# Optimization experiments

Hardware: AMD Instinct MI355X
Metric: run time of the kernel (lower is better)

Reference implementation:

```python
import jax, jax.numpy as jnp
import numpy as np

N = 100000
NEG_SLOPE = 0.2

def _leaky_relu(x, slope):
    return jnp.where(x >= 0, x, slope * x)

def _gat_layer(h_in, W, a_src, a_dst, b, src, dst, heads, out_ch):
    # h: [N, H, C]
    h = (h_in @ W).reshape(-1, heads, out_ch)
    alpha_src = (h * a_src).sum(-1)  # [N, H]
    alpha_dst = (h * a_dst).sum(-1)  # [N, H]
    e = _leaky_relu(alpha_src[src] + alpha_dst[dst], NEG_SLOPE)  # [E, H]
    # segment softmax over destination nodes
    m = jax.ops.segment_max(e, dst, num_segments=N)
    m = jnp.where(jnp.isfinite(m), m, 0.0)
    ex = jnp.exp(e - m[dst])
    denom = jax.ops.segment_sum(ex, dst, num_segments=N)
    attn = ex / (denom[dst] + 1e-16)  # [E, H]
    out = jax.ops.segment_sum(h[src] * attn[:, :, None], dst, num_segments=N)  # [N, H, C]
    return out.reshape(-1, heads * out_ch) + b

def setup_inputs() -> dict:
    key = jax.random.key(0)
    ks = jax.random.split(key, 10)
    F_in, H1, C1, n_cls = 512, 8, 8, 16
    E = 1600000
    x = jax.random.normal(ks[0], (N, F_in), dtype=jnp.float32)
    edge_index = jax.random.randint(ks[1], (2, E), 0, N, dtype=jnp.int64)
    s1 = 1.0 / np.sqrt(F_in)
    W1 = jax.random.uniform(ks[2], (F_in, H1 * C1), jnp.float32, -s1, s1)
    a1_src = jax.random.normal(ks[3], (H1, C1), dtype=jnp.float32) * 0.1
    a1_dst = jax.random.normal(ks[4], (H1, C1), dtype=jnp.float32) * 0.1
    b1 = jnp.zeros((H1 * C1,), jnp.float32)
    s2 = 1.0 / np.sqrt(H1 * C1)
    W2 = jax.random.uniform(ks[5], (H1 * C1, n_cls), jnp.float32, -s2, s2)
    a2_src = jax.random.normal(ks[6], (1, n_cls), dtype=jnp.float32) * 0.1
    a2_dst = jax.random.normal(ks[7], (1, n_cls), dtype=jnp.float32) * 0.1
    b2 = jnp.zeros((n_cls,), jnp.float32)
    return {"x": x, "edge_index": edge_index, "W1": W1, "a1_src": a1_src,
            "a1_dst": a1_dst, "b1": b1, "W2": W2, "a2_src": a2_src,
            "a2_dst": a2_dst, "b2": b2}

def reference(x, edge_index, W1, a1_src, a1_dst, b1, W2, a2_src, a2_dst, b2):
    # add self loops (GATConv default)
    loops = jnp.arange(N, dtype=edge_index.dtype)
    src = jnp.concatenate([edge_index[0], loops])
    dst = jnp.concatenate([edge_index[1], loops])
    h = _gat_layer(x, W1, a1_src, a1_dst, b1, src, dst, 8, 8)
    h = jax.nn.elu(h)
    out = _gat_layer(h, W2, a2_src, a2_dst, b2, src, dst, 1, 16)
    return jax.nn.log_softmax(out, axis=1)
```

## Files before the change

kernel.cpp:

```cpp
#include <hip/hip_runtime.h>
#include <math.h>

#define NEG_SLOPE 0.2f
#define BKT_SHIFT 8
#define BKT_RANGE 256
#define EPB 4096

typedef __attribute__((ext_vector_type(8))) short bf16x8;
typedef __attribute__((ext_vector_type(4))) float f32x4;

__device__ __forceinline__ float elu1(float x)  { return x > 0.f ? x : expm1f(x); }

__device__ __forceinline__ unsigned short f2bf(float f) {
  unsigned u = __float_as_uint(f);
  unsigned r = (u + 0x7FFFu + ((u >> 16) & 1u)) >> 16;
  return (unsigned short)r;
}
__device__ __forceinline__ float bflo(unsigned u) { return __uint_as_float(u << 16); }
__device__ __forceinline__ float bfhi(unsigned u) { return __uint_as_float(u & 0xFFFF0000u); }
__device__ __forceinline__ unsigned cvt_pk_bf16(float lo, float hi) {
  unsigned r;
  asm("v_cvt_pk_bf16_f32 %0, %1, %2" : "=v"(r) : "v"(lo), "v"(hi));
  return r;
}

__global__ __launch_bounds__(256) void k_cvtW_zero(const float* __restrict__ W,
                                                   unsigned short* __restrict__ Wt,
                                                   int* __restrict__ bucketCount) {
  int i = blockIdx.x * 256 + threadIdx.x;
  if (i < 1024) bucketCount[i] = 0;
  if (i >= 512 * 64) return;
  int k = i >> 6, c = i & 63;
  Wt[(size_t)c * 512 + k] = f2bf(W[i]);
}

__global__ __launch_bounds__(256) void k_gemm1_mfma(const float* __restrict__ x,
                                                    const unsigned short* __restrict__ Wt,
                                                    const float* __restrict__ a1s,
                                                    const float* __restrict__ a1d,
                                                    unsigned* __restrict__ hx,
                                                    unsigned* __restrict__ ef1dp, int N) {
  __shared__ __align__(16) float Sm[64 * 64];
  unsigned short* Bs = (unsigned short*)Sm;
  float* Asf = Sm;
  const int t = threadIdx.x;
  const int w = t >> 6;
  const int l = t & 63;
  const int fr = l & 15;
  const int fq = l >> 4;
  const int rowbase = blockIdx.x * 128;
  f32x4 acc[2][4] = {};

  const int r0g = rowbase + w * 32 + fr;
  const int r1g = r0g + 16;
  const bool v0 = r0g < N, v1 = r1g < N;
  const float* xr0 = x + (size_t)r0g * 512 + fq * 8;
  const float* xr1 = x + (size_t)r1g * 512 + fq * 8;

  for (int k0 = 0; k0 < 512; k0 += 64) {
#pragma unroll
    for (int rep = 0; rep < 2; ++rep) {
      int i = t + rep * 256;
      int c = i >> 3, ch = i & 7;
      uint4 v = *(const uint4*)(Wt + (size_t)c * 512 + k0 + ch * 8);
      *((uint4*)(Bs + c * 64 + (ch ^ (c & 7)) * 8)) = v;
    }
    bf16x8 a[2][2];
#pragma unroll
    for (int m = 0; m < 2; ++m) {
      const float* xr = m ? xr1 : xr0;
      bool vv = m ? v1 : v0;
#pragma unroll
      for (int ks = 0; ks < 2; ++ks) {
        float4 f0 = make_float4(0.f, 0.f, 0.f, 0.f), f1 = f0;
        if (vv) {
          f0 = *(const float4*)(xr + k0 + ks * 32);
          f1 = *(const float4*)(xr + k0 + ks * 32 + 4);
        }
        union { unsigned u[4]; bf16x8 v8; } un;
        un.u[0] = cvt_pk_bf16(f0.x, f0.y);
        un.u[1] = cvt_pk_bf16(f0.z, f0.w);
        un.u[2] = cvt_pk_bf16(f1.x, f1.y);
        un.u[3] = cvt_pk_bf16(f1.z, f1.w);
        a[m][ks] = un.v8;
      }
    }
    __syncthreads();
#pragma unroll
    for (int ks = 0; ks < 2; ++ks) {
      bf16x8 b[4];
#pragma unroll
      for (int n = 0; n < 4; ++n) {
        int c = n * 16 + fr;
        int ch = (ks * 4 + fq) ^ (c & 7);
        b[n] = *((const bf16x8*)(Bs + c * 64 + ch * 8));
      }
#pragma unroll
      for (int m = 0; m < 2; ++m)
#pragma unroll
        for (int n = 0; n < 4; ++n)
          acc[m][n] = __builtin_amdgcn_mfma_f32_16x16x32_bf16(a[m][ks], b[n], acc[m][n], 0, 0, 0);
    }
    __syncthreads();
  }

#pragma unroll
  for (int m = 0; m < 2; ++m) {
    if (m) __syncthreads();
#pragma unroll
    for (int reg = 0; reg < 4; ++reg) {
      int lrow = w * 16 + fq * 4 + reg;
#pragma unroll
      for (int n = 0; n < 4; ++n)
        Asf[lrow * 64 + n * 16 + fr] = acc[m][n][reg];
    }
    __syncthreads();
#pragma unroll
    for (int p = 0; p < 4; ++p) {
      int flat = p * 256 + t;
      int lrow = flat >> 4, j = flat & 15;
      int g = rowbase + ((lrow >> 4) << 5) + m * 16 + (lrow & 15);
      float4 f = *(float4*)(Asf + lrow * 64 + j * 4);
      unsigned u = __builtin_amdgcn_cvt_pk_fp8_f32(f.x, f.y, 0u, 0);
      u = __builtin_amdgcn_cvt_pk_fp8_f32(f.z, f.w, u, 1);
      if (g < N) hx[(size_t)g * 24 + 8 + j] = u;
    }
#pragma unroll
    for (int p = 0; p < 2; ++p) {
      int flat = p * 256 + t;
      int lrow = flat >> 3, hh = flat & 7;
      int g = rowbase + ((lrow >> 4) << 5) + m * 16 + (lrow & 15);
      float4 f0 = *(float4*)(Asf + lrow * 64 + hh * 8);
      float4 f1 = *(float4*)(Asf + lrow * 64 + hh * 8 + 4);
      const float* sa = a1s + hh * 8;
      const float* da = a1d + hh * 8;
      float ss = f0.x*sa[0]+f0.y*sa[1]+f0.z*sa[2]+f0.w*sa[3]
               + f1.x*sa[4]+f1.y*sa[5]+f1.z*sa[6]+f1.w*sa[7];
      float dd = f0.x*da[0]+f0.y*da[1]+f0.z*da[2]+f0.w*da[3]
               + f1.x*da[4]+f1.y*da[5]+f1.z*da[6]+f1.w*da[7];
      if (g < N) {
        hx[(size_t)g * 24 + hh] = cvt_pk_bf16(expf(ss), expf(NEG_SLOPE * ss));
        ef1dp[(size_t)g * 8 + hh] = cvt_pk_bf16(expf(dd), expf(NEG_SLOPE * dd));
      }
    }
  }
}

__global__ __launch_bounds__(256) void k_bhist(const int* __restrict__ dst,
                                               int* __restrict__ bucketCount,
                                               int E, int B) {
  __shared__ int h[512];
  int t = threadIdx.x;
  for (int i = t; i < B; i += 256) h[i] = 0;
  __syncthreads();
  int e0 = blockIdx.x * EPB;
#pragma unroll
  for (int i = 0; i < EPB / 256; ++i) {
    int e = e0 + i * 256 + t;
    if (e < E) atomicAdd(&h[dst[e] >> BKT_SHIFT], 1);
  }
  __syncthreads();
  for (int i = t; i < B; i += 256)
    if (h[i]) atomicAdd(bucketCount + i, h[i]);
}

__global__ __launch_bounds__(256) void k_bin(const int* __restrict__ src,
                                             const int* __restrict__ dst,
                                             const int* __restrict__ bucketCount,
                                             int* __restrict__ gCursorRel,
                                             unsigned* __restrict__ binned,
                                             int E, int B) {
  __shared__ int sc[512];
  __shared__ int hist[512];
  __shared__ int base[512];
  int t = threadIdx.x;
  sc[t]       = (t < B) ? bucketCount[t] : 0;
  sc[t + 256] = (t + 256 < B) ? bucketCount[t + 256] : 0;
  for (int i = t; i < 512; i += 256) hist[i] = 0;
  __syncthreads();
  for (int o = 1; o < 512; o <<= 1) {
    int a0 = (t >= o) ? sc[t - o] : 0;
    int a1 = (t + 256 >= o) ? sc[t + 256 - o] : 0;
    __syncthreads();
    sc[t] += a0;
    sc[t + 256] += a1;
    __syncthreads();
  }
  int e0 = blockIdx.x * EPB;
#pragma unroll
  for (int i = 0; i < EPB / 256; ++i) {
    int e = e0 + i * 256 + t;
    if (e < E) atomicAdd(&hist[dst[e] >> BKT_SHIFT], 1);
  }
  __syncthreads();
  for (int i = t; i < B; i += 256) {
    int c = hist[i];
    int excl = sc[i] - bucketCount[i];
    base[i] = c ? (excl + atomicAdd(gCursorRel + i, c)) : 0;
    hist[i] = 0;
  }
  __syncthreads();
#pragma unroll
  for (int i = 0; i < EPB / 256; ++i) {
    int e = e0 + i * 256 + t;
    if (e < E) {
      int d = dst[e];
      int b = d >> BKT_SHIFT;
      int r = atomicAdd(&hist[b], 1);
      binned[base[b] + r] = ((unsigned)(d & (BKT_RANGE - 1)) << 24) | (unsigned)src[e];
    }
  }
}

__global__ __launch_bounds__(256) void k_build(const int* __restrict__ bucketCount,
                                               const unsigned* __restrict__ binned,
                                               int* __restrict__ rowptr,
                                               int* __restrict__ deg,
                                               int* __restrict__ srt, int N, int B) {
  __shared__ int sc[512];
  __shared__ int ldeg[BKT_RANGE];
  __shared__ int sm[BKT_RANGE];
  __shared__ int lcur[BKT_RANGE];
  int t = threadIdx.x;
  int b = blockIdx.x;
  sc[t]       = (t < B) ? bucketCount[t] : 0;
  sc[t + 256] = (t + 256 < B) ? bucketCount[t + 256] : 0;
  ldeg[t] = 0;
  __syncthreads();
  for (int o = 1; o < 512; o <<= 1) {
    int a0 = (t >= o) ? sc[t - o] : 0;
    int a1 = (t + 256 >= o) ? sc[t + 256 - o] : 0;
    __syncthreads();
    sc[t] += a0;
    sc[t + 256] += a1;
    __syncthreads();
  }
  int eend = sc[b];
  int estart = eend - bucketCount[b];
  int nbase = b * BKT_RANGE;
  for (int e = estart + t; e < eend; e += 256)
    atomicAdd(&ldeg[binned[e] >> 24], 1);
  __syncthreads();
  int v = ldeg[t];
  sm[t] = v;
  __syncthreads();
  int acc = v;
#pragma unroll
  for (int o = 1; o < 256; o <<= 1) {
    int u = (t >= o) ? sm[t - o] : 0;
    __syncthreads();
    acc += u;
    sm[t] = acc;
    __syncthreads();
  }
  int excl = estart + acc - v;
  int node = nbase + t;
  if (node < N) {
    rowptr[node] = excl;
    deg[node] = v;
  }
  lcur[t] = excl;
  __syncthreads();
  for (int e = estart + t; e < eend; e += 256) {
    unsigned p = binned[e];
    int pos = atomicAdd(&lcur[p >> 24], 1);
    srt[pos] = (int)(p & 0xFFFFFFu);
  }
}

__global__ __launch_bounds__(256) void k_agg1f(const int* __restrict__ rowptr,
                                               const int* __restrict__ deg,
                                               const int* __restrict__ srt,
                                               const unsigned* __restrict__ hx,
                                               const unsigned* __restrict__ ef1dp,
                                               const float* __restrict__ b1,
                                               const float* __restrict__ W2,
                                               const float* __restrict__ a2s,
                                               const float* __restrict__ a2d,
                                               unsigned short* __restrict__ h2b,
                                               unsigned* __restrict__ ef2sp,
                                               float* __restrict__ ef2d, int N) {
  __shared__ float vsm[4][64];
  const int t = threadIdx.x;
  const int w = t >> 6;
  const int lane = t & 63;
  const int wid = blockIdx.x * 4 + w;
  const int slot = lane >> 4;
  const int c4 = lane & 15;
  const int h = c4 >> 1;
  float a2sr = a2s[c4];
  float a2dr = a2d[c4];
  float wreg[16];
#pragma unroll
  for (int m = 0; m < 16; ++m) wreg[m] = W2[(slot * 16 + m) * 16 + c4];
  float4 b1v = *(const float4*)(b1 + c4 * 4);
  if (wid >= N) return;
  const int d = wid;

  unsigned ddu = ef1dp[(size_t)d * 8 + h];
  float ddx = bflo(ddu), ddy = bfhi(ddu);
  unsigned es0 = hx[(size_t)d * 24 + h];
  unsigned sv = hx[(size_t)d * 24 + 8 + c4];
  float ex0 = fmaxf(bflo(es0) * ddx, bfhi(es0) * ddy);
  ex0 = (slot == 0) ? ex0 : 0.f;
  float a0 = ex0 * __builtin_amdgcn_cvt_f32_fp8(sv, 0);
  float a1 = ex0 * __builtin_amdgcn_cvt_f32_fp8(sv, 1);
  float a2 = ex0 * __builtin_amdgcn_cvt_f32_fp8(sv, 2);
  float a3 = ex0 * __builtin_amdgcn_cvt_f32_fp8(sv, 3);
  float den = ex0;

  int start = rowptr[d];
  int len = deg[d];
  for (int kb = 0; kb < len; kb += 64) {
    int li = kb + lane;
    int sreg = (li < len) ? srt[start + li] : 0;
    int nit = min(16, (len - kb + 3) >> 2);
#pragma unroll 4
    for (int it = 0; it < nit; ++it) {
      int idx = kb + it * 4 + slot;
      int s = __shfl(sreg, it * 4 + slot);
      bool valid = idx < len;
      unsigned es = hx[(size_t)s * 24 + h];
      unsigned hv = hx[(size_t)s * 24 + 8 + c4];
      float ex = fmaxf(bflo(es) * ddx, bfhi(es) * ddy);
      ex = valid ? ex : 0.f;
      a0 = fmaf(ex, __builtin_amdgcn_cvt_f32_fp8(hv, 0), a0);
      a1 = fmaf(ex, __builtin_amdgcn_cvt_f32_fp8(hv, 1), a1);
      a2 = fmaf(ex, __builtin_amdgcn_cvt_f32_fp8(hv, 2), a2);
      a3 = fmaf(ex, __builtin_amdgcn_cvt_f32_fp8(hv, 3), a3);
      den += ex;
    }
  }
#pragma unroll
  for (int o = 16; o < 64; o <<= 1) {
    a0 += __shfl_xor(a0, o);
    a1 += __shfl_xor(a1, o);
    a2 += __shfl_xor(a2, o);
    a3 += __shfl_xor(a3, o);
    den += __shfl_xor(den, o);
  }
  float rden = 1.f / (den + 1e-16f);
  if (slot == 0) {
    float4 vv;
    vv.x = elu1(a0 * rden + b1v.x);
    vv.y = elu1(a1 * rden + b1v.y);
    vv.z = elu1(a2 * rden + b1v.z);
    vv.w = elu1(a3 * rden + b1v.w);
    *(float4*)&vsm[w][c4 * 4] = vv;
  }
  float partial = 0.f;
#pragma unroll
  for (int m = 0; m < 16; ++m) partial = fmaf(vsm[w][slot * 16 + m], wreg[m], partial);
  float qs = partial * a2sr;
  float qd = partial * a2dr;
#pragma unroll
  for (int o = 1; o < 64; o <<= 1) {
    qs += __shfl_xor(qs, o);
    qd += __shfl_xor(qd, o);
  }
  float p2 = partial + __shfl_down(partial, 32);
  float hcv = p2 + __shfl_down(p2, 16);
  if (lane < 16) h2b[(size_t)d * 16 + c4] = f2bf(hcv);
  if (lane == 0) {
    ef2sp[d] = cvt_pk_bf16(expf(qs), expf(NEG_SLOPE * qs));
    *(float2*)(ef2d + (size_t)d * 2) = make_float2(expf(qd), expf(NEG_SLOPE * qd));
  }
}

__global__ __launch_bounds__(256) void k_agg2(const int* __restrict__ rowptr,
                                              const int* __restrict__ deg,
                                              const int* __restrict__ srt,
                                              const unsigned* __restrict__ ef2sp,
                                              const float* __restrict__ ef2d,
                                              const unsigned short* __restrict__ h2b,
                                              const float* __restrict__ b2,
                                              float* __restrict__ out, int N) {
  const int t = threadIdx.x;
  const int lane = t & 63;
  const int wid = (blockIdx.x * 256 + t) >> 6;
  const int slot = lane >> 2;
  const int cg = lane & 3;
  float4 b2v = *(const float4*)(b2 + cg * 4);
  if (wid >= N) return;
  const int d = wid;
  float2 ddp = *(const float2*)(ef2d + (size_t)d * 2);
  unsigned ps0 = ef2sp[d];
  uint2 sv = *(const uint2*)(h2b + (size_t)d * 16 + cg * 4);
  float ex0 = fmaxf(bflo(ps0) * ddp.x, bfhi(ps0) * ddp.y);
  ex0 = (slot == 0) ? ex0 : 0.f;
  float a0 = ex0 * bflo(sv.x), a1 = ex0 * bfhi(sv.x);
  float a2 = ex0 * bflo(sv.y), a3 = ex0 * bfhi(sv.y);
  float den = ex0;

  int start = rowptr[d];
  int len = deg[d];
  for (int kb = 0; kb < len; kb += 64) {
    int li = kb + lane;
    int sreg = (li < len) ? srt[start + li] : 0;
    int nit = min(4, (len - kb + 15) >> 4);
#pragma unroll 4
    for (int it = 0; it < nit; ++it) {
      int idx = kb + it * 16 + slot;
      int s = __shfl(sreg, it * 16 + slot);
      bool valid = idx < len;
      unsigned ps = ef2sp[s];
      uint2 hv = *(const uint2*)(h2b + (size_t)s * 16 + cg * 4);
      float ex = fmaxf(bflo(ps) * ddp.x, bfhi(ps) * ddp.y);
      ex = valid ? ex : 0.f;
      a0 = fmaf(ex, bflo(hv.x), a0);
      a1 = fmaf(ex, bfhi(hv.x), a1);
      a2 = fmaf(ex, bflo(hv.y), a2);
      a3 = fmaf(ex, bfhi(hv.y), a3);
      den += ex;
    }
  }
#pragma unroll
  for (int o = 4; o < 64; o <<= 1) {
    a0 += __shfl_xor(a0, o);
    a1 += __shfl_xor(a1, o);
    a2 += __shfl_xor(a2, o);
    a3 += __shfl_xor(a3, o);
    den += __shfl_xor(den, o);
  }
  float rden = 1.f / (den + 1e-16f);
  float v0 = a0 * rden + b2v.x;
  float v1 = a1 * rden + b2v.y;
  float v2 = a2 * rden + b2v.z;
  float v3 = a3 * rden + b2v.w;
  float m = fmaxf(fmaxf(v0, v1), fmaxf(v2, v3));
  m = fmaxf(m, __shfl_xor(m, 1));
  m = fmaxf(m, __shfl_xor(m, 2));
  float s = expf(v0 - m) + expf(v1 - m) + expf(v2 - m) + expf(v3 - m);
  s += __shfl_xor(s, 1);
  s += __shfl_xor(s, 2);
  float lse = m + logf(s);
  if (lane < 4) {
    float4 o4 = make_float4(v0 - lse, v1 - lse, v2 - lse, v3 - lse);
    *(float4*)(out + (size_t)d * 16 + cg * 4) = o4;
  }
}

extern "C" void kernel_launch(void* const* d_in, const int* in_sizes, int n_in,
                              void* d_out, int out_size, void* d_ws, size_t ws_size,
                              hipStream_t stream) {
  const float* x    = (const float*)d_in[0];
  const int*   ei   = (const int*)d_in[1];
  const float* W1   = (const float*)d_in[2];
  const float* a1s  = (const float*)d_in[3];
  const float* a1d  = (const float*)d_in[4];
  const float* b1   = (const float*)d_in[5];
  const float* W2   = (const float*)d_in[6];
  const float* a2s  = (const float*)d_in[7];
  const float* a2d  = (const float*)d_in[8];
  const float* b2   = (const float*)d_in[9];
  float* out = (float*)d_out;

  const int N = in_sizes[0] / 512;
  const int E = in_sizes[1] / 2;
  const int* src = ei;
  const int* dst = ei + E;
  const int B = (N + BKT_RANGE - 1) >> BKT_SHIFT;
  const int EB = (E + EPB - 1) / EPB;

  float* w = (float*)d_ws;
  float* ef2d = w;  w += (size_t)N * 2;
  unsigned* ef1dp = (unsigned*)w;  w += (size_t)N * 8;
  unsigned* ef2sp = (unsigned*)w;  w += (size_t)N;
  unsigned* hx    = (unsigned*)w;  w += (size_t)N * 24;
  unsigned short* h2b = (unsigned short*)w;  w += (size_t)N * 8;
  unsigned short* Wt  = (unsigned short*)w;  w += 512 * 64 / 2;
  int* iw = (int*)w;
  int* deg         = iw;  iw += N;
  int* rowptr      = iw;  iw += N;
  int* bucketCount = iw;  iw += 512;
  int* gCursorRel  = iw;  iw += 512;
  int* srt         = iw;  iw += E;
  unsigned* binned = (unsigned*)iw;  iw += E;

  k_cvtW_zero<<<(512 * 64 + 255) / 256, 256, 0, stream>>>(W1, Wt, bucketCount);

  k_bhist<<<EB, 256, 0, stream>>>(dst, bucketCount, E, B);
  k_bin<<<EB, 256, 0, stream>>>(src, dst, bucketCount, gCursorRel, binned, E, B);
  k_build<<<B, 256, 0, stream>>>(bucketCount, binned, rowptr, deg, srt, N, B);

  k_gemm1_mfma<<<(N + 127) / 128, 256, 0, stream>>>(x, Wt, a1s, a1d, hx, ef1dp, N);
  k_agg1f<<<(N + 3) / 4, 256, 0, stream>>>(rowptr, deg, srt, hx, ef1dp,
                                           b1, W2, a2s, a2d, h2b, ef2sp, ef2d, N);

  k_agg2<<<(N + 3) / 4, 256, 0, stream>>>(rowptr, deg, srt, ef2sp, ef2d, h2b, b2, out, N);
}
```

Measured before the change: 212.0 us.

## Pad node records to 128/64 bytes and fold W conversion into histogram kernel

Per-node layer-1 data (exp src/dst pairs plus fp8 features) is packed into one 128-byte record, and layer-2 data (src exp pair, dst exp pair, bf16 features) into one 64-byte record. Each gathered neighbour then touches a single aligned cache line instead of several separate arrays. The W1-to-bf16 transpose is merged into the histogram kernel as extra blocks, and the bucket counter zeroing becomes a memset, removing one kernel launch. The cost is more padded memory footprint, and the agg1 gather still only reads part of each 128-byte record.

```diff
diff --git a/kernel.cpp b/kernel.cpp
--- a/kernel.cpp
+++ b/kernel.cpp
@@ -24,22 +24,11 @@
   return r;
 }
 
-__global__ __launch_bounds__(256) void k_cvtW_zero(const float* __restrict__ W,
-                                                   unsigned short* __restrict__ Wt,
-                                                   int* __restrict__ bucketCount) {
-  int i = blockIdx.x * 256 + threadIdx.x;
-  if (i < 1024) bucketCount[i] = 0;
-  if (i >= 512 * 64) return;
-  int k = i >> 6, c = i & 63;
-  Wt[(size_t)c * 512 + k] = f2bf(W[i]);
-}
-
 __global__ __launch_bounds__(256) void k_gemm1_mfma(const float* __restrict__ x,
                                                     const unsigned short* __restrict__ Wt,
                                                     const float* __restrict__ a1s,
                                                     const float* __restrict__ a1d,
-                                                    unsigned* __restrict__ hx,
-                                                    unsigned* __restrict__ ef1dp, int N) {
+                                                    unsigned* __restrict__ hx, int N) {
   __shared__ __align__(16) float Sm[64 * 64];
   unsigned short* Bs = (unsigned short*)Sm;
   float* Asf = Sm;
@@ -123,7 +112,7 @@
       float4 f = *(float4*)(Asf + lrow * 64 + j * 4);
       unsigned u = __builtin_amdgcn_cvt_pk_fp8_f32(f.x, f.y, 0u, 0);
       u = __builtin_amdgcn_cvt_pk_fp8_f32(f.z, f.w, u, 1);
-      if (g < N) hx[(size_t)g * 24 + 8 + j] = u;
+      if (g < N) hx[(size_t)g * 32 + 16 + j] = u;
     }
 #pragma unroll
     for (int p = 0; p < 2; ++p) {
@@ -139,21 +128,32 @@
       float dd = f0.x*da[0]+f0.y*da[1]+f0.z*da[2]+f0.w*da[3]
                + f1.x*da[4]+f1.y*da[5]+f1.z*da[6]+f1.w*da[7];
       if (g < N) {
-        hx[(size_t)g * 24 + hh] = cvt_pk_bf16(expf(ss), expf(NEG_SLOPE * ss));
-        ef1dp[(size_t)g * 8 + hh] = cvt_pk_bf16(expf(dd), expf(NEG_SLOPE * dd));
+        hx[(size_t)g * 32 + hh]     = cvt_pk_bf16(expf(ss), expf(NEG_SLOPE * ss));
+        hx[(size_t)g * 32 + 8 + hh] = cvt_pk_bf16(expf(dd), expf(NEG_SLOPE * dd));
       }
     }
   }
 }
 
-__global__ __launch_bounds__(256) void k_bhist(const int* __restrict__ dst,
-                                               int* __restrict__ bucketCount,
-                                               int E, int B) {
+__global__ __launch_bounds__(256) void k_bhist_cvtW(const int* __restrict__ dst,
+                                                    int* __restrict__ bucketCount,
+                                                    const float* __restrict__ W,
+                                                    unsigned short* __restrict__ Wt,
+                                                    int E, int B, int EB) {
+  int blk = blockIdx.x;
+  int t = threadIdx.x;
+  if (blk >= EB) {
+    int i = (blk - EB) * 256 + t;
+    if (i < 512 * 64) {
+      int k = i >> 6, c = i & 63;
+      Wt[(size_t)c * 512 + k] = f2bf(W[i]);
+    }
+    return;
+  }
   __shared__ int h[512];
-  int t = threadIdx.x;
   for (int i = t; i < B; i += 256) h[i] = 0;
   __syncthreads();
-  int e0 = blockIdx.x * EPB;
+  int e0 = blk * EPB;
 #pragma unroll
   for (int i = 0; i < EPB / 256; ++i) {
     int e = e0 + i * 256 + t;
@@ -272,14 +272,11 @@
                                                const int* __restrict__ deg,
                                                const int* __restrict__ srt,
                                                const unsigned* __restrict__ hx,
-                                               const unsigned* __restrict__ ef1dp,
                                                const float* __restrict__ b1,
                                                const float* __restrict__ W2,
                                                const float* __restrict__ a2s,
                                                const float* __restrict__ a2d,
-                                               unsigned short* __restrict__ h2b,
-                                               unsigned* __restrict__ ef2sp,
-                                               float* __restrict__ ef2d, int N) {
+                                               unsigned* __restrict__ h2x, int N) {
   __shared__ float vsm[4][64];
   const int t = threadIdx.x;
   const int w = t >> 6;
@@ -297,10 +294,10 @@
   if (wid >= N) return;
   const int d = wid;
 
-  unsigned ddu = ef1dp[(size_t)d * 8 + h];
+  unsigned ddu = hx[(size_t)d * 32 + 8 + h];
   float ddx = bflo(ddu), ddy = bfhi(ddu);
-  unsigned es0 = hx[(size_t)d * 24 + h];
-  unsigned sv = hx[(size_t)d * 24 + 8 + c4];
+  unsigned es0 = hx[(size_t)d * 32 + h];
+  unsigned sv = hx[(size_t)d * 32 + 16 + c4];
   float ex0 = fmaxf(bflo(es0) * ddx, bfhi(es0) * ddy);
   ex0 = (slot == 0) ? ex0 : 0.f;
   float a0 = ex0 * __builtin_amdgcn_cvt_f32_fp8(sv, 0);
@@ -320,8 +317,8 @@
       int idx = kb + it * 4 + slot;
       int s = __shfl(sreg, it * 4 + slot);
       bool valid = idx < len;
-      unsigned es = hx[(size_t)s * 24 + h];
-      unsigned hv = hx[(size_t)s * 24 + 8 + c4];
+      unsigned es = hx[(size_t)s * 32 + h];
+      unsigned hv = hx[(size_t)s * 32 + 16 + c4];
       float ex = fmaxf(bflo(es) * ddx, bfhi(es) * ddy);
       ex = valid ? ex : 0.f;
       a0 = fmaf(ex, __builtin_amdgcn_cvt_f32_fp8(hv, 0), a0);
@@ -360,19 +357,18 @@
   }
   float p2 = partial + __shfl_down(partial, 32);
   float hcv = p2 + __shfl_down(p2, 16);
-  if (lane < 16) h2b[(size_t)d * 16 + c4] = f2bf(hcv);
+  if (lane < 16)
+    ((unsigned short*)h2x)[(size_t)d * 32 + 8 + c4] = f2bf(hcv);
   if (lane == 0) {
-    ef2sp[d] = cvt_pk_bf16(expf(qs), expf(NEG_SLOPE * qs));
-    *(float2*)(ef2d + (size_t)d * 2) = make_float2(expf(qd), expf(NEG_SLOPE * qd));
+    h2x[(size_t)d * 16] = cvt_pk_bf16(expf(qs), expf(NEG_SLOPE * qs));
+    *(float2*)(h2x + (size_t)d * 16 + 2) = make_float2(expf(qd), expf(NEG_SLOPE * qd));
   }
 }
 
 __global__ __launch_bounds__(256) void k_agg2(const int* __restrict__ rowptr,
                                               const int* __restrict__ deg,
                                               const int* __restrict__ srt,
-                                              const unsigned* __restrict__ ef2sp,
-                                              const float* __restrict__ ef2d,
-                                              const unsigned short* __restrict__ h2b,
+                                              const unsigned* __restrict__ h2x,
                                               const float* __restrict__ b2,
                                               float* __restrict__ out, int N) {
   const int t = threadIdx.x;
@@ -383,9 +379,9 @@
   float4 b2v = *(const float4*)(b2 + cg * 4);
   if (wid >= N) return;
   const int d = wid;
-  float2 ddp = *(const float2*)(ef2d + (size_t)d * 2);
-  unsigned ps0 = ef2sp[d];
-  uint2 sv = *(const uint2*)(h2b + (size_t)d * 16 + cg * 4);
+  float2 ddp = *(const float2*)(h2x + (size_t)d * 16 + 2);
+  unsigned ps0 = h2x[(size_t)d * 16];
+  uint2 sv = *(const uint2*)(h2x + (size_t)d * 16 + 4 + cg * 2);
   float ex0 = fmaxf(bflo(ps0) * ddp.x, bfhi(ps0) * ddp.y);
   ex0 = (slot == 0) ? ex0 : 0.f;
   float a0 = ex0 * bflo(sv.x), a1 = ex0 * bfhi(sv.x);
@@ -403,8 +399,8 @@
       int idx = kb + it * 16 + slot;
       int s = __shfl(sreg, it * 16 + slot);
       bool valid = idx < len;
-      unsigned ps = ef2sp[s];
-      uint2 hv = *(const uint2*)(h2b + (size_t)s * 16 + cg * 4);
+      unsigned ps = h2x[(size_t)s * 16];
+      uint2 hv = *(const uint2*)(h2x + (size_t)s * 16 + 4 + cg * 2);
       float ex = fmaxf(bflo(ps) * ddp.x, bfhi(ps) * ddp.y);
       ex = valid ? ex : 0.f;
       a0 = fmaf(ex, bflo(hv.x), a0);
@@ -463,12 +459,9 @@
   const int EB = (E + EPB - 1) / EPB;
 
   float* w = (float*)d_ws;
-  float* ef2d = w;  w += (size_t)N * 2;
-  unsigned* ef1dp = (unsigned*)w;  w += (size_t)N * 8;
-  unsigned* ef2sp = (unsigned*)w;  w += (size_t)N;
-  unsigned* hx    = (unsigned*)w;  w += (size_t)N * 24;
-  unsigned short* h2b = (unsigned short*)w;  w += (size_t)N * 8;
-  unsigned short* Wt  = (unsigned short*)w;  w += 512 * 64 / 2;
+  unsigned* hx  = (unsigned*)w;             w += (size_t)N * 32;
+  unsigned* h2x = (unsigned*)w;             w += (size_t)N * 16;
+  unsigned short* Wt = (unsigned short*)w;  w += 512 * 64 / 2;
   int* iw = (int*)w;
   int* deg         = iw;  iw += N;
   int* rowptr      = iw;  iw += N;
@@ -477,15 +470,15 @@
   int* srt         = iw;  iw += E;
   unsigned* binned = (unsigned*)iw;  iw += E;
 
-  k_cvtW_zero<<<(512 * 64 + 255) / 256, 256, 0, stream>>>(W1, Wt, bucketCount);
-
-  k_bhist<<<EB, 256, 0, stream>>>(dst, bucketCount, E, B);
+  hipMemsetAsync(bucketCount, 0, 1024 * sizeof(int), stream);
+
+  k_bhist_cvtW<<<EB + 128, 256, 0, stream>>>(dst, bucketCount, W1, Wt, E, B, EB);
   k_bin<<<EB, 256, 0, stream>>>(src, dst, bucketCount, gCursorRel, binned, E, B);
   k_build<<<B, 256, 0, stream>>>(bucketCount, binned, rowptr, deg, srt, N, B);
 
-  k_gemm1_mfma<<<(N + 127) / 128, 256, 0, stream>>>(x, Wt, a1s, a1d, hx, ef1dp, N);
-  k_agg1f<<<(N + 3) / 4, 256, 0, stream>>>(rowptr, deg, srt, hx, ef1dp,
-                                           b1, W2, a2s, a2d, h2b, ef2sp, ef2d, N);
-
-  k_agg2<<<(N + 3) / 4, 256, 0, stream>>>(rowptr, deg, srt, ef2sp, ef2d, h2b, b2, out, N);
-}
+  k_gemm1_mfma<<<(N + 127) / 128, 256, 0, stream>>>(x, Wt, a1s, a1d, hx, N);
+  k_agg1f<<<(N + 3) / 4, 256, 0, stream>>>(rowptr, deg, srt, hx,
+                                           b1, W2, a2s, a2d, h2x, N);
+
+  k_agg2<<<(N + 3) / 4, 256, 0, stream>>>(rowptr, deg, srt, h2x, b2, out, N);
+}
```

New measurement: 211.0 us. Within noise of the previous version (-0.5%).
